# Optimization experiments

Measured on AMD Instinct MI355X. Metric: run time of the kernel, lower is better.

Reference implementation:

```python
import jax, jax.numpy as jnp
import numpy as np

HH, WW = 56, 56          # input resolution
WS, SS = 7, 3            # window size, shift size
HEADS = 6
DIM = 192
HID = 768
B = 32
EPS = 1e-5


def _rel_pos_index(ws):
    coords = np.stack(np.meshgrid(np.arange(ws), np.arange(ws), indexing='ij'))  # [2,ws,ws]
    cf = coords.reshape(2, -1)                       # [2,N]
    rel = cf[:, :, None] - cf[:, None, :]            # [2,N,N]
    rel = rel.transpose(1, 2, 0).copy()              # [N,N,2]
    rel[:, :, 0] += ws - 1
    rel[:, :, 1] += ws - 1
    rel[:, :, 0] *= 2 * ws - 1
    return rel.sum(-1)                               # [N,N] int


def _attn_mask(H, W, ws, ss):
    img = np.zeros((H, W))
    cnt = 0
    sl = (slice(0, -ws), slice(-ws, -ss), slice(-ss, None))
    for hs in sl:
        for wsl in sl:
            img[hs, wsl] = cnt
            cnt += 1
    mw = img.reshape(H // ws, ws, W // ws, ws).transpose(0, 2, 1, 3).reshape(-1, ws * ws)  # [nW,N]
    diff = mw[:, None, :] - mw[:, :, None]           # matches unsqueeze(1)-unsqueeze(2)
    return np.where(diff != 0, -100.0, 0.0).astype(np.float32)  # [nW,N,N]


_RPI = jnp.asarray(_rel_pos_index(WS))               # [49,49] int
_MASK = jnp.asarray(_attn_mask(HH, WW, WS, SS))      # [64,49,49] f32


def _ln(v, g, b):
    mu = v.mean(-1, keepdims=True)
    var = v.var(-1, keepdims=True)
    return (v - mu) / jnp.sqrt(var + EPS) * g + b


def setup_inputs() -> dict:
    key = jax.random.key(0)
    ks = jax.random.split(key, 10)
    s = 0.02
    return {
        'x': jax.random.normal(ks[0], (B, HH * WW, DIM), jnp.float32),
        'norm1_g': jnp.ones((DIM,), jnp.float32),
        'norm1_b': jnp.zeros((DIM,), jnp.float32),
        'qkv_w': jax.random.normal(ks[1], (DIM, 3 * DIM), jnp.float32) * s,
        'qkv_b': jax.random.normal(ks[2], (3 * DIM,), jnp.float32) * s,
        'rpb_table': jax.random.normal(ks[3], (169, HEADS), jnp.float32) * s,
        'proj_w': jax.random.normal(ks[4], (DIM, DIM), jnp.float32) * s,
        'proj_b': jax.random.normal(ks[5], (DIM,), jnp.float32) * s,
        'norm2_g': jnp.ones((DIM,), jnp.float32),
        'norm2_b': jnp.zeros((DIM,), jnp.float32),
        'fc1_w': jax.random.normal(ks[6], (DIM, HID), jnp.float32) * s,
        'fc1_b': jax.random.normal(ks[7], (HID,), jnp.float32) * s,
        'fc2_w': jax.random.normal(ks[8], (HID, DIM), jnp.float32) * s,
        'fc2_b': jax.random.normal(ks[9], (DIM,), jnp.float32) * s,
    }


def reference(x, norm1_g, norm1_b, qkv_w, qkv_b, rpb_table, proj_w, proj_b,
              norm2_g, norm2_b, fc1_w, fc1_b, fc2_w, fc2_b):
    Bn, L, C = x.shape
    h, ws, ss = HEADS, WS, SS
    d = C // h
    scale = d ** -0.5
    N = ws * ws
    nWh, nWw = HH // ws, WW // ws

    shortcut = x
    xh = _ln(x, norm1_g, norm1_b).reshape(Bn, HH, WW, C)
    xh = jnp.roll(xh, (-ss, -ss), axis=(1, 2))                       # cyclic shift
    # window partition -> (B*nW, N, C)
    xw = xh.reshape(Bn, nWh, ws, nWw, ws, C).transpose(0, 1, 3, 2, 4, 5).reshape(-1, N, C)

    qkv = (xw @ qkv_w + qkv_b).reshape(-1, N, 3, h, d).transpose(2, 0, 3, 1, 4)
    q, k, v = qkv[0] * scale, qkv[1], qkv[2]                         # (B_,h,N,d)
    attn = jnp.einsum('bhnd,bhmd->bhnm', q, k)                       # (B_,h,N,N)

    bias = rpb_table[_RPI.reshape(-1)].reshape(N, N, h).transpose(2, 0, 1)  # (h,N,N)
    attn = attn + bias[None]
    nW = _MASK.shape[0]
    attn = attn.reshape(Bn, nW, h, N, N) + _MASK[None, :, None]
    attn = jax.nn.softmax(attn.reshape(-1, h, N, N), axis=-1)

    out = jnp.einsum('bhnm,bhmd->bhnd', attn, v).transpose(0, 2, 1, 3).reshape(-1, N, C)
    out = out @ proj_w + proj_b
    # window reverse
    out = out.reshape(Bn, nWh, nWw, ws, ws, C).transpose(0, 1, 3, 2, 4, 5).reshape(Bn, HH, WW, C)
    out = jnp.roll(out, (ss, ss), axis=(1, 2)).reshape(Bn, L, C)     # reverse shift

    x1 = shortcut + out
    y = _ln(x1, norm2_g, norm2_b)
    y = jax.nn.gelu(y @ fc1_w + fc1_b, approximate=False)
    y = y @ fc2_w + fc2_b
    return x1 + y
```

## Files before the change

### kernel.cpp

```cpp
#include <hip/hip_runtime.h>
#include <cmath>

typedef __bf16  v8bf  __attribute__((ext_vector_type(8)));
typedef float   v4f   __attribute__((ext_vector_type(4)));

#define HH 56
#define WW2 56
#define SS 3
#define HEADS 6
#define DIM 192
#define HID 768
#define NTOK 49
#define NWIN 2048
#define MTOT (NWIN * NTOK)
#define SCALE 0.17677669529663687f

__device__ __forceinline__ void async_cp16(const __bf16* g, __bf16* l) {
    __builtin_amdgcn_global_load_lds(
        (const __attribute__((address_space(1))) void*)g,
        (__attribute__((address_space(3))) void*)l,
        16, 0, 0);
}

__device__ __forceinline__ void wg_barrier() {
    __builtin_amdgcn_sched_barrier(0);
    __builtin_amdgcn_s_barrier();
    __builtin_amdgcn_sched_barrier(0);
}
#define WAIT_LGKM0() asm volatile("s_waitcnt lgkmcnt(0)" ::: "memory")
#define WAIT_VM(n)   asm volatile("s_waitcnt vmcnt(" #n ")" ::: "memory")

__device__ __forceinline__ float fast_gelu(float x) {
    float z = fabsf(x) * 0.70710678118654752f;
    float t = __builtin_amdgcn_rcpf(1.f + 0.3275911f * z);
    float poly = t * (0.254829592f + t * (-0.284496736f +
                 t * (1.421413741f + t * (-1.453152027f + t * 1.061405429f))));
    float er = 1.f - poly * __expf(-z * z);
    er = (x < 0.f) ? -er : er;
    return 0.5f * x * (1.f + er);
}

__global__ void k_transpose(const float* __restrict__ in, __bf16* __restrict__ out,
                            int K, int N) {
    int idx = blockIdx.x * 256 + threadIdx.x;
    if (idx >= K * N) return;
    int n = idx / K, k = idx - n * K;
    out[idx] = (__bf16)in[k * N + n];
}

__global__ void k_prep_fc1(const float* __restrict__ w, __bf16* __restrict__ o) {
    int idx = blockIdx.x * 256 + threadIdx.x;
    if (idx >= HID * DIM) return;
    int n = idx / DIM, rem = idx - n * DIM;
    int b16 = rem >> 3, j = rem & 7;
    int k = 8 * (b16 ^ (n & 7)) + j;
    o[idx] = (__bf16)w[k * HID + n];
}

__global__ void k_prep_fc2(const float* __restrict__ w, __bf16* __restrict__ o) {
    int idx = blockIdx.x * 256 + threadIdx.x;
    if (idx >= HID * DIM) return;
    int hc = idx / (192 * 32);
    int rem = idx - hc * 192 * 32;
    int n = rem >> 5, k = rem & 31;
    o[idx] = (__bf16)w[(hc * 32 + k) * DIM + n];
}

__global__ void k_bias(const float* __restrict__ rpb, float* __restrict__ bt) {
    int type = blockIdx.x, h = blockIdx.y;
    for (int idx = threadIdx.x; idx < 4096; idx += 256) {
        int m = idx >> 6, n = idx & 63;
        float v;
        if (m >= 49) v = -1e9f;
        else if (n >= 49) v = 0.f;
        else {
            int ni = n / 7, nj = n % 7, mi = m / 7, mj = m % 7;
            v = rpb[((ni - mi + 6) * 13 + (nj - mj + 6)) * 6 + h];
            int rin = (type & 2) ? ((ni < 4) ? 1 : 2) : 0;
            int rjn = (type & 1) ? ((nj < 4) ? 1 : 2) : 0;
            int rim = (type & 2) ? ((mi < 4) ? 1 : 2) : 0;
            int rjm = (type & 1) ? ((mj < 4) ? 1 : 2) : 0;
            if (rin * 3 + rjn != rim * 3 + rjm) v -= 100.f;
        }
        bt[((size_t)(type * HEADS + h) * 64 + m) * 64 + n] = v;
    }
}

__global__ __launch_bounds__(256) void k_ln1win(const float* __restrict__ x,
                                                const float* __restrict__ g,
                                                const float* __restrict__ bt,
                                                __bf16* __restrict__ xw) {
    int wv = threadIdx.x >> 6, lane = threadIdx.x & 63;
    int t = blockIdx.x * 4 + wv;
    int w = t / NTOK, p = t - w * NTOK;
    int b = w >> 6, wi = w & 63;
    int i = (wi >> 3) * 7 + p / 7;
    int j = (wi & 7) * 7 + p % 7;
    int io = i + SS; if (io >= HH) io -= HH;
    int jo = j + SS; if (jo >= WW2) jo -= WW2;
    const float* src = x + ((size_t)(b * 3136 + io * 56 + jo)) * DIM;
    float v0 = src[lane], v1 = src[lane + 64], v2 = src[lane + 128];
    float s = v0 + v1 + v2, s2 = v0 * v0 + v1 * v1 + v2 * v2;
    #pragma unroll
    for (int off = 1; off < 64; off <<= 1) {
        s  += __shfl_xor(s, off);
        s2 += __shfl_xor(s2, off);
    }
    float mu = s * (1.f / 192.f);
    float rstd = rsqrtf(s2 * (1.f / 192.f) - mu * mu + 1e-5f);
    __bf16* dst = xw + (size_t)t * DIM;
    dst[lane]       = (__bf16)((v0 - mu) * rstd * g[lane]       + bt[lane]);
    dst[lane + 64]  = (__bf16)((v1 - mu) * rstd * g[lane + 64]  + bt[lane + 64]);
    dst[lane + 128] = (__bf16)((v2 - mu) * rstd * g[lane + 128] + bt[lane + 128]);
}

template<int KDIM, int NDIM, int MODE>
__global__ __launch_bounds__(256) void k_gemm128(const __bf16* __restrict__ A,
                                                 const __bf16* __restrict__ Wt,
                                                 const float* __restrict__ bias,
                                                 __bf16* __restrict__ outb,
                                                 const float* __restrict__ x1in,
                                                 float* __restrict__ outf,
                                                 const float* __restrict__ xres) {
    __shared__ __bf16 lA[2][128 * 32];
    __shared__ __bf16 lB[2][128 * 32];
    const int tid = threadIdx.x;
    const int m0 = blockIdx.x * 128, n0 = blockIdx.y * 128;
    const int wv = tid >> 6, lane = tid & 63;
    const int wm = (wv >> 1) * 64, wn = (wv & 1) * 64;
    const int lrow = lane & 15, lq = lane >> 4;
    const int grow = tid >> 2, gkc = (tid & 3) * 8;

    auto stage = [&](int kk, int b) {
        #pragma unroll
        for (int c = 0; c < 2; c++) {
            int r = grow + c * 64;
            async_cp16(A + (size_t)(m0 + r) * KDIM + kk + gkc, lA[b] + tid * 8 + c * 2048);
            int rb = n0 + r;
            if (NDIM % 128) rb = (rb < NDIM) ? rb : (NDIM - 1);
            async_cp16(Wt + (size_t)rb * KDIM + kk + gkc, lB[b] + tid * 8 + c * 2048);
        }
    };
    stage(0, 0);
    stage(32, 1);

    v4f acc[4][4] = {};
    #pragma unroll
    for (int kk = 0; kk < KDIM; kk += 32) {
        const int b = (kk >> 5) & 1;
        if (kk + 32 < KDIM) { WAIT_VM(4); } else { WAIT_VM(0); }
        wg_barrier();
        v8bf af[4], bf[4];
        #pragma unroll
        for (int i = 0; i < 4; i++) {
            af[i] = *(const v8bf*)(lA[b] + (wm + i * 16 + lrow) * 32 + lq * 8);
            bf[i] = *(const v8bf*)(lB[b] + (wn + i * 16 + lrow) * 32 + lq * 8);
        }
        #pragma unroll
        for (int i = 0; i < 4; i++)
        #pragma unroll
        for (int j = 0; j < 4; j++)
            acc[i][j] = __builtin_amdgcn_mfma_f32_16x16x32_bf16(af[i], bf[j], acc[i][j], 0, 0, 0);
        wg_barrier();
        if (kk + 64 < KDIM) stage(kk + 64, b);
    }
    #pragma unroll
    for (int i = 0; i < 4; i++)
    #pragma unroll
    for (int j = 0; j < 4; j++) {
        int col = n0 + wn + j * 16 + lrow;
        if (NDIM % 128 && col >= NDIM) continue;
        float bv = bias[col];
        #pragma unroll
        for (int r = 0; r < 4; r++) {
            int row = m0 + wm + i * 16 + lq * 4 + r;
            float v = acc[i][j][r] + bv;
            if (MODE == 0) {
                __bf16* kbp = outb + (size_t)MTOT * DIM;
                __bf16* vbp = kbp + (size_t)MTOT * DIM;
                int which = col / DIM, rem = col - which * DIM;
                int hh = rem >> 5, d = rem & 31;
                int w = row / NTOK, p = row - w * NTOK;
                size_t off = ((size_t)(w * HEADS + hh) * NTOK + p) * 32 + d;
                if (which == 0)      outb[off] = (__bf16)(v * SCALE);
                else if (which == 1) kbp[off] = (__bf16)v;
                else                 vbp[off] = (__bf16)v;
            } else {
                int w = row / NTOK, p = row - w * NTOK;
                int bimg = w >> 6, wi = w & 63;
                int ii = (wi >> 3) * 7 + p / 7;
                int jj = (wi & 7) * 7 + p % 7;
                int io = ii + SS; if (io >= HH) io -= HH;
                int jo = jj + SS; if (jo >= WW2) jo -= WW2;
                size_t o = ((size_t)(bimg * 3136 + io * 56 + jo)) * DIM + col;
                outf[o] = v + xres[o];
            }
        }
    }
}

__global__ __launch_bounds__(64) void k_attn_mfma(const __bf16* __restrict__ qb,
                                                  const float* __restrict__ bias_tab,
                                                  __bf16* __restrict__ ao) {
    __shared__ __bf16 Pl[64 * 72];
    __shared__ __bf16 VTl[32 * 72];
    const __bf16* kb = qb + (size_t)MTOT * DIM;
    const __bf16* vb = kb + (size_t)MTOT * DIM;
    int wh = blockIdx.x;
    int w = wh / HEADS, h = wh - w * HEADS;
    int lane = threadIdx.x & 63;
    int c = lane & 15, q = lane >> 4;
    const size_t base = (size_t)wh * (NTOK * 32);

    for (int idx = lane; idx < 32 * 16; idx += 64)
        VTl[(idx >> 4) * 72 + 48 + (idx & 15)] = (__bf16)0.f;
    #pragma unroll
    for (int it = 0; it < 4; it++) {
        int idx = it * 64 + lane;
        if (idx < NTOK * 4) {
            int t = idx >> 2, d0 = (idx & 3) * 8;
            v8bf vv = *(const v8bf*)(vb + base + t * 32 + d0);
            #pragma unroll
            for (int ii = 0; ii < 8; ii++) VTl[(d0 + ii) * 72 + t] = vv[ii];
        }
    }
    v8bf af[4], bf[4];
    #pragma unroll
    for (int rt = 0; rt < 4; rt++) {
        int t = rt * 16 + c; t = (t > 48) ? 48 : t;
        af[rt] = *(const v8bf*)(qb + base + t * 32 + q * 8);
        bf[rt] = *(const v8bf*)(kb + base + t * 32 + q * 8);
    }
    v4f S[4][4] = {};
    #pragma unroll
    for (int rt = 0; rt < 4; rt++)
    #pragma unroll
    for (int ct = 0; ct < 4; ct++)
        S[rt][ct] = __builtin_amdgcn_mfma_f32_16x16x32_bf16(af[rt], bf[ct], S[rt][ct], 0, 0, 0);
    int wi = w & 63;
    int type = (((wi >> 3) == 7) ? 2 : 0) + (((wi & 7) == 7) ? 1 : 0);
    const float* bt = bias_tab + (size_t)(type * HEADS + h) * 4096;
    #pragma unroll
    for (int rt = 0; rt < 4; rt++)
    #pragma unroll
    for (int ct = 0; ct < 4; ct++) {
        v4f bv = *(const v4f*)(bt + (ct * 16 + c) * 64 + rt * 16 + q * 4);
        S[rt][ct] += bv;
    }
    v4f mx4[4], inv4[4];
    #pragma unroll
    for (int rt = 0; rt < 4; rt++) {
        v4f m;
        #pragma unroll
        for (int r = 0; r < 4; r++)
            m[r] = fmaxf(fmaxf(S[rt][0][r], S[rt][1][r]), fmaxf(S[rt][2][r], S[rt][3][r]));
        #pragma unroll
        for (int off = 1; off < 16; off <<= 1) {
            #pragma unroll
            for (int r = 0; r < 4; r++) m[r] = fmaxf(m[r], __shfl_xor(m[r], off));
        }
        mx4[rt] = m;
    }
    #pragma unroll
    for (int rt = 0; rt < 4; rt++) {
        v4f dsum = {};
        #pragma unroll
        for (int ct = 0; ct < 4; ct++) {
            #pragma unroll
            for (int r = 0; r < 4; r++) {
                float e = __expf(S[rt][ct][r] - mx4[rt][r]);
                dsum[r] += e;
                Pl[(rt * 16 + q * 4 + r) * 72 + ct * 16 + c] = (__bf16)e;
            }
        }
        #pragma unroll
        for (int off = 1; off < 16; off <<= 1) {
            #pragma unroll
            for (int r = 0; r < 4; r++) dsum[r] += __shfl_xor(dsum[r], off);
        }
        #pragma unroll
        for (int r = 0; r < 4; r++) inv4[rt][r] = 1.f / dsum[r];
    }
    __syncthreads();
    v4f O[4][2] = {};
    #pragma unroll
    for (int k2 = 0; k2 < 2; k2++) {
        v8bf pa[4], pb[2];
        #pragma unroll
        for (int rt = 0; rt < 4; rt++)
            pa[rt] = *(const v8bf*)(Pl + (rt * 16 + c) * 72 + k2 * 32 + q * 8);
        #pragma unroll
        for (int ct = 0; ct < 2; ct++)
            pb[ct] = *(const v8bf*)(VTl + (ct * 16 + c) * 72 + k2 * 32 + q * 8);
        #pragma unroll
        for (int rt = 0; rt < 4; rt++)
        #pragma unroll
        for (int ct = 0; ct < 2; ct++)
            O[rt][ct] = __builtin_amdgcn_mfma_f32_16x16x32_bf16(pa[rt], pb[ct], O[rt][ct], 0, 0, 0);
    }
    __bf16* aop = ao + (size_t)(w * NTOK) * DIM + h * 32;
    #pragma unroll
    for (int rt = 0; rt < 4; rt++)
    #pragma unroll
    for (int r = 0; r < 4; r++) {
        int row = rt * 16 + q * 4 + r;
        if (row < NTOK) {
            #pragma unroll
            for (int ct = 0; ct < 2; ct++)
                aop[(size_t)row * DIM + ct * 16 + c] = (__bf16)(O[rt][ct][r] * inv4[rt][r]);
        }
    }
}

__global__ __launch_bounds__(256, 4) void k_mlp_fused(
        const float* __restrict__ x1,
        const float* __restrict__ n2g, const float* __restrict__ n2b,
        const __bf16* __restrict__ fc1S, const float* __restrict__ fc1b,
        const __bf16* __restrict__ fc2S, const float* __restrict__ fc2b,
        float* __restrict__ out) {
    __shared__ __align__(16) char sm[40704];
    char* bufX = sm;
    char* lH   = sm + 12288;
    char* bufY = sm + 24576;
    float* lB1 = (float*)(sm + 36864);
    float* lB2 = (float*)(sm + 39936);
    const int tid = threadIdx.x;
    const int wv = tid >> 6, lane = tid & 63;
    const int lrow = lane & 15, lq = lane >> 4;
    const int m0 = blockIdx.x * 64;

    #pragma unroll
    for (int p = 0; p < 3; ++p)
        async_cp16(fc1S + p * 2048 + tid * 8, (__bf16*)bufY + p * 2048 + tid * 8);

    #pragma unroll
    for (int p = 0; p < 3; ++p) lB1[p * 256 + tid] = fc1b[p * 256 + tid];
    if (tid < 192) lB2[tid] = fc2b[tid];

    {
        float g0 = n2g[lane], g1 = n2g[lane + 64], g2 = n2g[lane + 128];
        float b0 = n2b[lane], b1 = n2b[lane + 64], b2 = n2b[lane + 128];
        #pragma unroll 4
        for (int it = 0; it < 16; ++it) {
            int row = wv * 16 + it;
            const float* src = x1 + (size_t)(m0 + row) * DIM;
            float v0 = src[lane], v1 = src[lane + 64], v2 = src[lane + 128];
            float s = v0 + v1 + v2, s2 = v0 * v0 + v1 * v1 + v2 * v2;
            #pragma unroll
            for (int off = 1; off < 64; off <<= 1) {
                s  += __shfl_xor(s, off);
                s2 += __shfl_xor(s2, off);
            }
            float mu = s * (1.f / 192.f);
            float rstd = rsqrtf(s2 * (1.f / 192.f) - mu * mu + 1e-5f);
            char* rb = sm + row * 384;
            int xo = (row & 7) << 4;
            *(__bf16*)(rb + ((lane * 2)       ^ xo)) = (__bf16)((v0 - mu) * rstd * g0 + b0);
            *(__bf16*)(rb + ((lane * 2 + 128) ^ xo)) = (__bf16)((v1 - mu) * rstd * g1 + b1);
            *(__bf16*)(rb + ((lane * 2 + 256) ^ xo)) = (__bf16)((v2 - mu) * rstd * g2 + b2);
        }
    }
    WAIT_LGKM0();
    wg_barrier();

    const int wm  = (wv >> 1) * 32;
    const int wc1 = (wv & 1) * 16;
    const int wn  = (wv & 1) * 96;
    v8bf afr[2][6];
    #pragma unroll
    for (int i = 0; i < 2; ++i) {
        int ra = wm + i * 16 + lrow;
        #pragma unroll
        for (int ks = 0; ks < 6; ++ks)
            afr[i][ks] = *(const v8bf*)(sm + ra * 384 + ((ks * 64 + lq * 16) ^ ((ra & 7) << 4)));
    }
    WAIT_LGKM0();
    wg_barrier();

    #pragma unroll
    for (int p = 0; p < 3; ++p)
        async_cp16(fc2S + p * 2048 + tid * 8, (__bf16*)bufX + p * 2048 + tid * 8);

    v4f oacc[2][6] = {};
    for (int hc = 0; hc < 24; ++hc) {
        int hn = hc + 1; if (hn == 24) hn = 0;
        v4f hacc[2] = {};
        __builtin_amdgcn_s_setprio(1);
        #pragma unroll
        for (int ks = 0; ks < 6; ++ks) {
            int rw = wc1 + lrow;
            v8bf bw = *(const v8bf*)(bufY + rw * 384 + ((ks * 64 + lq * 16) ^ ((rw & 7) << 4)));
            #pragma unroll
            for (int i = 0; i < 2; ++i)
                hacc[i] = __builtin_amdgcn_mfma_f32_16x16x32_bf16(afr[i][ks], bw, hacc[i], 0, 0, 0);
        }
        __builtin_amdgcn_s_setprio(0);
        {
            float bv = lB1[hc * 32 + wc1 + lrow];
            #pragma unroll
            for (int i = 0; i < 2; ++i)
            #pragma unroll
            for (int r = 0; r < 4; ++r) {
                int row = wm + i * 16 + lq * 4 + r;
                int col = wc1 + lrow;
                float hv = hacc[i][r] + bv;
                *(__bf16*)(lH + row * 64 + col * 2) = (__bf16)fast_gelu(hv);
            }
        }
        WAIT_LGKM0();
        wg_barrier();
        {
            const __bf16* s1 = fc1S + (size_t)hn * (32 * 192);
            #pragma unroll
            for (int p = 0; p < 3; ++p)
                async_cp16(s1 + p * 2048 + tid * 8, (__bf16*)bufY + p * 2048 + tid * 8);
        }
        WAIT_VM(3);
        wg_barrier();
        __builtin_amdgcn_s_setprio(1);
        {
            v8bf pa[2], pb[6];
            #pragma unroll
            for (int i = 0; i < 2; ++i) {
                int ra = wm + i * 16 + lrow;
                pa[i] = *(const v8bf*)(lH + ra * 64 + lq * 16);
            }
            #pragma unroll
            for (int j = 0; j < 6; ++j) {
                int rw = wn + j * 16 + lrow;
                pb[j] = *(const v8bf*)(bufX + rw * 64 + lq * 16);
            }
            #pragma unroll
            for (int i = 0; i < 2; ++i)
            #pragma unroll
            for (int j = 0; j < 6; ++j)
                oacc[i][j] = __builtin_amdgcn_mfma_f32_16x16x32_bf16(pa[i], pb[j], oacc[i][j], 0, 0, 0);
        }
        __builtin_amdgcn_s_setprio(0);
        WAIT_LGKM0();
        wg_barrier();
        {
            const __bf16* s2 = fc2S + (size_t)hn * (192 * 32);
            #pragma unroll
            for (int p = 0; p < 3; ++p)
                async_cp16(s2 + p * 2048 + tid * 8, (__bf16*)bufX + p * 2048 + tid * 8);
        }
        WAIT_VM(3);
        wg_barrier();
    }
    WAIT_VM(0);
    #pragma unroll
    for (int i = 0; i < 2; ++i)
    #pragma unroll
    for (int j = 0; j < 6; ++j) {
        int col = wn + j * 16 + lrow;
        float bv = lB2[col];
        #pragma unroll
        for (int r = 0; r < 4; ++r) {
            int row = m0 + wm + i * 16 + lq * 4 + r;
            size_t o = (size_t)row * DIM + col;
            out[o] = oacc[i][j][r] + bv + x1[o];
        }
    }
}

extern "C" void kernel_launch(void* const* d_in, const int* in_sizes, int n_in,
                              void* d_out, int out_size, void* d_ws, size_t ws_size,
                              hipStream_t stream) {
    const float* x      = (const float*)d_in[0];
    const float* n1g    = (const float*)d_in[1];
    const float* n1b    = (const float*)d_in[2];
    const float* qkv_w  = (const float*)d_in[3];
    const float* qkv_b  = (const float*)d_in[4];
    const float* rpb    = (const float*)d_in[5];
    const float* proj_w = (const float*)d_in[6];
    const float* proj_b = (const float*)d_in[7];
    const float* n2g    = (const float*)d_in[8];
    const float* n2b    = (const float*)d_in[9];
    const float* fc1_w  = (const float*)d_in[10];
    const float* fc1_b  = (const float*)d_in[11];
    const float* fc2_w  = (const float*)d_in[12];
    const float* fc2_b  = (const float*)d_in[13];
    float* outp = (float*)d_out;

    char* ws = (char*)d_ws;
    const size_t SZA = (size_t)MTOT * DIM * 2;
    __bf16* xw = (__bf16*)ws;
    __bf16* qb = (__bf16*)(ws + SZA);
    float*  x1 = (float*)(ws + SZA);
    char* wbase = ws + 4 * SZA;
    __bf16* qkvT  = (__bf16*)wbase;
    __bf16* projT = qkvT + 576 * 192;
    __bf16* fc1S  = projT + 192 * 192;
    __bf16* fc2S  = fc1S + 768 * 192;
    float*  btab  = (float*)(fc2S + 768 * 192);

    k_transpose<<<(192 * 576 + 255) / 256, 256, 0, stream>>>(qkv_w, qkvT, 192, 576);
    k_transpose<<<(192 * 192 + 255) / 256, 256, 0, stream>>>(proj_w, projT, 192, 192);
    k_prep_fc1<<<(768 * 192 + 255) / 256, 256, 0, stream>>>(fc1_w, fc1S);
    k_prep_fc2<<<(768 * 192 + 255) / 256, 256, 0, stream>>>(fc2_w, fc2S);
    k_bias<<<dim3(4, HEADS), 256, 0, stream>>>(rpb, btab);

    k_ln1win<<<MTOT / 4, 256, 0, stream>>>(x, n1g, n1b, xw);

    k_gemm128<192, 576, 0><<<dim3(MTOT / 128, 5), 256, 0, stream>>>(
        xw, qkvT, qkv_b, qb, nullptr, nullptr, nullptr);

    k_attn_mfma<<<NWIN * HEADS, 64, 0, stream>>>(qb, btab, xw);

    k_gemm128<192, 192, 1><<<dim3(MTOT / 128, 2), 256, 0, stream>>>(
        xw, projT, proj_b, nullptr, nullptr, x1, x);

    k_mlp_fused<<<MTOT / 64, 256, 0, stream>>>(
        x1, n2g, n2b, fc1S, fc1_b, fc2S, fc2_b, outp);
}
```

Measured before the change: 524.6 us.

## Rewrite fused MLP as single-wave blocks reading weights from global

```diff
diff --git a/kernel.cpp b/kernel.cpp
--- a/kernel.cpp
+++ b/kernel.cpp
@@ -27,14 +27,12 @@
     __builtin_amdgcn_s_barrier();
     __builtin_amdgcn_sched_barrier(0);
 }
-#define WAIT_LGKM0() asm volatile("s_waitcnt lgkmcnt(0)" ::: "memory")
 #define WAIT_VM(n)   asm volatile("s_waitcnt vmcnt(" #n ")" ::: "memory")
 
 __device__ __forceinline__ float fast_gelu(float x) {
     float z = fabsf(x) * 0.70710678118654752f;
-    float t = __builtin_amdgcn_rcpf(1.f + 0.3275911f * z);
-    float poly = t * (0.254829592f + t * (-0.284496736f +
-                 t * (1.421413741f + t * (-1.453152027f + t * 1.061405429f))));
+    float t = __builtin_amdgcn_rcpf(1.f + 0.47047f * z);
+    float poly = t * (0.3480242f + t * (-0.0958798f + t * 0.7478556f));
     float er = 1.f - poly * __expf(-z * z);
     er = (x < 0.f) ? -er : er;
     return 0.5f * x * (1.f + er);
@@ -46,24 +44,6 @@
     if (idx >= K * N) return;
     int n = idx / K, k = idx - n * K;
     out[idx] = (__bf16)in[k * N + n];
-}
-
-__global__ void k_prep_fc1(const float* __restrict__ w, __bf16* __restrict__ o) {
-    int idx = blockIdx.x * 256 + threadIdx.x;
-    if (idx >= HID * DIM) return;
-    int n = idx / DIM, rem = idx - n * DIM;
-    int b16 = rem >> 3, j = rem & 7;
-    int k = 8 * (b16 ^ (n & 7)) + j;
-    o[idx] = (__bf16)w[k * HID + n];
-}
-
-__global__ void k_prep_fc2(const float* __restrict__ w, __bf16* __restrict__ o) {
-    int idx = blockIdx.x * 256 + threadIdx.x;
-    if (idx >= HID * DIM) return;
-    int hc = idx / (192 * 32);
-    int rem = idx - hc * 192 * 32;
-    int n = rem >> 5, k = rem & 31;
-    o[idx] = (__bf16)w[(hc * 32 + k) * DIM + n];
 }
 
 __global__ void k_bias(const float* __restrict__ rpb, float* __restrict__ bt) {
@@ -312,37 +292,22 @@
     }
 }
 
-__global__ __launch_bounds__(256, 4) void k_mlp_fused(
+__global__ __launch_bounds__(64) void k_mlp_fused(
         const float* __restrict__ x1,
         const float* __restrict__ n2g, const float* __restrict__ n2b,
-        const __bf16* __restrict__ fc1S, const float* __restrict__ fc1b,
-        const __bf16* __restrict__ fc2S, const float* __restrict__ fc2b,
+        const __bf16* __restrict__ fc1T, const float* __restrict__ fc1b,
+        const __bf16* __restrict__ fc2T, const float* __restrict__ fc2b,
         float* __restrict__ out) {
-    __shared__ __align__(16) char sm[40704];
-    char* bufX = sm;
-    char* lH   = sm + 12288;
-    char* bufY = sm + 24576;
-    float* lB1 = (float*)(sm + 36864);
-    float* lB2 = (float*)(sm + 39936);
-    const int tid = threadIdx.x;
-    const int wv = tid >> 6, lane = tid & 63;
+    __shared__ __align__(16) char sm[14848];
+    char* lH = sm + 12288;
+    const int lane = threadIdx.x;
     const int lrow = lane & 15, lq = lane >> 4;
-    const int m0 = blockIdx.x * 64;
-
-    #pragma unroll
-    for (int p = 0; p < 3; ++p)
-        async_cp16(fc1S + p * 2048 + tid * 8, (__bf16*)bufY + p * 2048 + tid * 8);
-
-    #pragma unroll
-    for (int p = 0; p < 3; ++p) lB1[p * 256 + tid] = fc1b[p * 256 + tid];
-    if (tid < 192) lB2[tid] = fc2b[tid];
+    const int m0 = blockIdx.x * 32;
 
     {
         float g0 = n2g[lane], g1 = n2g[lane + 64], g2 = n2g[lane + 128];
         float b0 = n2b[lane], b1 = n2b[lane + 64], b2 = n2b[lane + 128];
-        #pragma unroll 4
-        for (int it = 0; it < 16; ++it) {
-            int row = wv * 16 + it;
+        for (int row = 0; row < 32; ++row) {
             const float* src = x1 + (size_t)(m0 + row) * DIM;
             float v0 = src[lane], v1 = src[lane + 64], v2 = src[lane + 128];
             float s = v0 + v1 + v2, s2 = v0 * v0 + v1 * v1 + v2 * v2;
@@ -360,104 +325,60 @@
             *(__bf16*)(rb + ((lane * 2 + 256) ^ xo)) = (__bf16)((v2 - mu) * rstd * g2 + b2);
         }
     }
-    WAIT_LGKM0();
-    wg_barrier();
-
-    const int wm  = (wv >> 1) * 32;
-    const int wc1 = (wv & 1) * 16;
-    const int wn  = (wv & 1) * 96;
+
     v8bf afr[2][6];
     #pragma unroll
     for (int i = 0; i < 2; ++i) {
-        int ra = wm + i * 16 + lrow;
+        int ra = i * 16 + lrow;
         #pragma unroll
         for (int ks = 0; ks < 6; ++ks)
             afr[i][ks] = *(const v8bf*)(sm + ra * 384 + ((ks * 64 + lq * 16) ^ ((ra & 7) << 4)));
     }
-    WAIT_LGKM0();
-    wg_barrier();
-
-    #pragma unroll
-    for (int p = 0; p < 3; ++p)
-        async_cp16(fc2S + p * 2048 + tid * 8, (__bf16*)bufX + p * 2048 + tid * 8);
-
-    v4f oacc[2][6] = {};
+
+    const __bf16* f1p = fc1T + (size_t)lrow * 192 + lq * 8;
+    const __bf16* f2p = fc2T + (size_t)lrow * 768 + lq * 8;
+
+    v4f oacc[2][12] = {};
     for (int hc = 0; hc < 24; ++hc) {
-        int hn = hc + 1; if (hn == 24) hn = 0;
-        v4f hacc[2] = {};
-        __builtin_amdgcn_s_setprio(1);
+        v4f hacc[2][2] = {};
         #pragma unroll
         for (int ks = 0; ks < 6; ++ks) {
-            int rw = wc1 + lrow;
-            v8bf bw = *(const v8bf*)(bufY + rw * 384 + ((ks * 64 + lq * 16) ^ ((rw & 7) << 4)));
-            #pragma unroll
-            for (int i = 0; i < 2; ++i)
-                hacc[i] = __builtin_amdgcn_mfma_f32_16x16x32_bf16(afr[i][ks], bw, hacc[i], 0, 0, 0);
-        }
-        __builtin_amdgcn_s_setprio(0);
-        {
-            float bv = lB1[hc * 32 + wc1 + lrow];
-            #pragma unroll
-            for (int i = 0; i < 2; ++i)
-            #pragma unroll
-            for (int r = 0; r < 4; ++r) {
-                int row = wm + i * 16 + lq * 4 + r;
-                int col = wc1 + lrow;
-                float hv = hacc[i][r] + bv;
-                *(__bf16*)(lH + row * 64 + col * 2) = (__bf16)fast_gelu(hv);
+            v8bf bw0 = *(const v8bf*)(f1p + (size_t)(hc * 32) * 192 + ks * 32);
+            v8bf bw1 = *(const v8bf*)(f1p + (size_t)(hc * 32 + 16) * 192 + ks * 32);
+            #pragma unroll
+            for (int i = 0; i < 2; ++i) {
+                hacc[i][0] = __builtin_amdgcn_mfma_f32_16x16x32_bf16(afr[i][ks], bw0, hacc[i][0], 0, 0, 0);
+                hacc[i][1] = __builtin_amdgcn_mfma_f32_16x16x32_bf16(afr[i][ks], bw1, hacc[i][1], 0, 0, 0);
             }
         }
-        WAIT_LGKM0();
-        wg_barrier();
-        {
-            const __bf16* s1 = fc1S + (size_t)hn * (32 * 192);
-            #pragma unroll
-            for (int p = 0; p < 3; ++p)
-                async_cp16(s1 + p * 2048 + tid * 8, (__bf16*)bufY + p * 2048 + tid * 8);
-        }
-        WAIT_VM(3);
-        wg_barrier();
-        __builtin_amdgcn_s_setprio(1);
-        {
-            v8bf pa[2], pb[6];
-            #pragma unroll
-            for (int i = 0; i < 2; ++i) {
-                int ra = wm + i * 16 + lrow;
-                pa[i] = *(const v8bf*)(lH + ra * 64 + lq * 16);
-            }
-            #pragma unroll
-            for (int j = 0; j < 6; ++j) {
-                int rw = wn + j * 16 + lrow;
-                pb[j] = *(const v8bf*)(bufX + rw * 64 + lq * 16);
-            }
-            #pragma unroll
-            for (int i = 0; i < 2; ++i)
-            #pragma unroll
-            for (int j = 0; j < 6; ++j)
-                oacc[i][j] = __builtin_amdgcn_mfma_f32_16x16x32_bf16(pa[i], pb[j], oacc[i][j], 0, 0, 0);
-        }
-        __builtin_amdgcn_s_setprio(0);
-        WAIT_LGKM0();
-        wg_barrier();
-        {
-            const __bf16* s2 = fc2S + (size_t)hn * (192 * 32);
-            #pragma unroll
-            for (int p = 0; p < 3; ++p)
-                async_cp16(s2 + p * 2048 + tid * 8, (__bf16*)bufX + p * 2048 + tid * 8);
-        }
-        WAIT_VM(3);
-        wg_barrier();
-    }
-    WAIT_VM(0);
-    #pragma unroll
-    for (int i = 0; i < 2; ++i)
-    #pragma unroll
-    for (int j = 0; j < 6; ++j) {
-        int col = wn + j * 16 + lrow;
-        float bv = lB2[col];
+        float bv0 = fc1b[hc * 32 + lrow];
+        float bv1 = fc1b[hc * 32 + 16 + lrow];
+        #pragma unroll
+        for (int i = 0; i < 2; ++i)
         #pragma unroll
         for (int r = 0; r < 4; ++r) {
-            int row = m0 + wm + i * 16 + lq * 4 + r;
+            int row = i * 16 + lq * 4 + r;
+            *(__bf16*)(lH + row * 80 + lrow * 2)      = (__bf16)fast_gelu(hacc[i][0][r] + bv0);
+            *(__bf16*)(lH + row * 80 + 32 + lrow * 2) = (__bf16)fast_gelu(hacc[i][1][r] + bv1);
+        }
+        v8bf pa0 = *(const v8bf*)(lH + lrow * 80 + lq * 16);
+        v8bf pa1 = *(const v8bf*)(lH + (16 + lrow) * 80 + lq * 16);
+        #pragma unroll
+        for (int j = 0; j < 12; ++j) {
+            v8bf pb = *(const v8bf*)(f2p + (size_t)(j * 16) * 768 + hc * 32);
+            oacc[0][j] = __builtin_amdgcn_mfma_f32_16x16x32_bf16(pa0, pb, oacc[0][j], 0, 0, 0);
+            oacc[1][j] = __builtin_amdgcn_mfma_f32_16x16x32_bf16(pa1, pb, oacc[1][j], 0, 0, 0);
+        }
+    }
+    #pragma unroll
+    for (int j = 0; j < 12; ++j) {
+        int col = j * 16 + lrow;
+        float bv = fc2b[col];
+        #pragma unroll
+        for (int i = 0; i < 2; ++i)
+        #pragma unroll
+        for (int r = 0; r < 4; ++r) {
+            int row = m0 + i * 16 + lq * 4 + r;
             size_t o = (size_t)row * DIM + col;
             out[o] = oacc[i][j][r] + bv + x1[o];
         }
@@ -491,14 +412,14 @@
     char* wbase = ws + 4 * SZA;
     __bf16* qkvT  = (__bf16*)wbase;
     __bf16* projT = qkvT + 576 * 192;
-    __bf16* fc1S  = projT + 192 * 192;
-    __bf16* fc2S  = fc1S + 768 * 192;
-    float*  btab  = (float*)(fc2S + 768 * 192);
+    __bf16* fc1T  = projT + 192 * 192;
+    __bf16* fc2T  = fc1T + 768 * 192;
+    float*  btab  = (float*)(fc2T + 192 * 768);
 
     k_transpose<<<(192 * 576 + 255) / 256, 256, 0, stream>>>(qkv_w, qkvT, 192, 576);
     k_transpose<<<(192 * 192 + 255) / 256, 256, 0, stream>>>(proj_w, projT, 192, 192);
-    k_prep_fc1<<<(768 * 192 + 255) / 256, 256, 0, stream>>>(fc1_w, fc1S);
-    k_prep_fc2<<<(768 * 192 + 255) / 256, 256, 0, stream>>>(fc2_w, fc2S);
+    k_transpose<<<(192 * 768 + 255) / 256, 256, 0, stream>>>(fc1_w, fc1T, 192, 768);
+    k_transpose<<<(768 * 192 + 255) / 256, 256, 0, stream>>>(fc2_w, fc2T, 768, 192);
     k_bias<<<dim3(4, HEADS), 256, 0, stream>>>(rpb, btab);
 
     k_ln1win<<<MTOT / 4, 256, 0, stream>>>(x, n1g, n1b, xw);
@@ -511,6 +432,6 @@
     k_gemm128<192, 192, 1><<<dim3(MTOT / 128, 2), 256, 0, stream>>>(
         xw, projT, proj_b, nullptr, nullptr, x1, x);
 
-    k_mlp_fused<<<MTOT / 64, 256, 0, stream>>>(
-        x1, n2g, n2b, fc1S, fc1_b, fc2S, fc2_b, outp);
-}
+    k_mlp_fused<<<MTOT / 32, 64, 0, stream>>>(
+        x1, n2g, n2b, fc1T, fc1_b, fc2T, fc2_b, outp);
+}
```

After: 709.8 us. 35.3% more time.
